# Kernel tuning notes

Measured on AMD Instinct MI355X. Metric: run time of the kernel, lower is better.

The kernel has to match this reference:

```python
import jax, jax.numpy as jnp
import numpy as np

B, C, H, W = 8, 256, 128, 128
HEADS, WS = 8, 8
SHIFT = WS // 2  # type=='W' -> shift_size = window_size//2 in this repo
N = WS * WS


def _rel_pos_index(ws):
    coords = np.stack(np.meshgrid(np.arange(ws), np.arange(ws), indexing='ij')).reshape(2, -1)
    rel = (coords[:, :, None] - coords[:, None, :]).transpose(1, 2, 0)  # N,N,2
    rel[:, :, 0] += ws - 1
    rel[:, :, 1] += ws - 1
    rel[:, :, 0] *= 2 * ws - 1
    return rel.sum(-1)  # (N,N) ints in [0,(2ws-1)^2)


def _attn_mask(h, w, ws, shift):
    img = np.zeros((h, w), np.int32)
    cnt = 0
    for hs in (slice(0, -ws), slice(-ws, -shift), slice(-shift, None)):
        for wsl in (slice(0, -ws), slice(-ws, -shift), slice(-shift, None)):
            img[hs, wsl] = cnt
            cnt += 1
    m = img.reshape(h // ws, ws, w // ws, ws).transpose(0, 2, 1, 3).reshape(-1, ws * ws)
    diff = m[:, None, :] - m[:, :, None]
    return np.where(diff != 0, -100.0, 0.0).astype(np.float32)  # (nW,N,N)


def _ln(x, w, b, eps=1e-5):
    mu = jnp.mean(x, -1, keepdims=True)
    var = jnp.mean(jnp.square(x - mu), -1, keepdims=True)
    return (x - mu) * jax.lax.rsqrt(var + eps) * w + b


def setup_inputs() -> dict:
    key = jax.random.key(0)
    ks = jax.random.split(key, 10)
    s = 0.02
    return {
        'x': jax.random.normal(ks[0], (B, C, H, W), jnp.float32),
        'ln1_w': jnp.ones((C,), jnp.float32),
        'ln1_b': jnp.zeros((C,), jnp.float32),
        'qkv_w': jax.random.normal(ks[1], (3 * C, C), jnp.float32) * s,
        'qkv_b': jnp.zeros((3 * C,), jnp.float32),
        'rel_bias': jax.random.normal(ks[2], ((2 * WS - 1) ** 2, HEADS), jnp.float32) * s,
        'proj_w': jax.random.normal(ks[3], (C, C), jnp.float32) * s,
        'proj_b': jnp.zeros((C,), jnp.float32),
        'ln2_w': jnp.ones((C,), jnp.float32),
        'ln2_b': jnp.zeros((C,), jnp.float32),
        'fc1_w': jax.random.normal(ks[4], (4 * C, C), jnp.float32) * s,
        'fc1_b': jnp.zeros((4 * C,), jnp.float32),
        'fc2_w': jax.random.normal(ks[5], (C, 4 * C), jnp.float32) * s,
        'fc2_b': jnp.zeros((C,), jnp.float32),
    }


def reference(x, ln1_w, ln1_b, qkv_w, qkv_b, rel_bias, proj_w, proj_b,
              ln2_w, ln2_b, fc1_w, fc1_b, fc2_w, fc2_b):
    b, c, h, w = x.shape
    hd = c // HEADS
    scale = hd ** -0.5
    nW = (h // WS) * (w // WS)

    t = x.transpose(0, 2, 3, 1).reshape(b, h * w, c)  # b (hw) c
    shortcut = t
    t = _ln(t, ln1_w, ln1_b).reshape(b, h, w, c)
    t = jnp.roll(t, (-SHIFT, -SHIFT), axis=(1, 2))  # cyclic shift
    # window partition -> (b*nW, N, c)
    win = t.reshape(b, h // WS, WS, w // WS, WS, c).transpose(0, 1, 3, 2, 4, 5).reshape(b * nW, N, c)

    qkv = (win @ qkv_w.T + qkv_b).reshape(b * nW, N, 3, HEADS, hd).transpose(2, 0, 3, 1, 4)
    q, k, v = qkv[0], qkv[1], qkv[2]  # (b*nW, heads, N, hd)
    attn = jnp.einsum('bhnd,bhmd->bhnm', q * scale, k)
    rpi = jnp.asarray(_rel_pos_index(WS))
    bias = rel_bias[rpi.reshape(-1)].reshape(N, N, HEADS).transpose(2, 0, 1)  # (heads,N,N)
    attn = attn + bias[None]
    mask = jnp.asarray(_attn_mask(h, w, WS, SHIFT))  # (nW,N,N)
    attn = attn.reshape(b, nW, HEADS, N, N) + mask[None, :, None]
    attn = jax.nn.softmax(attn, axis=-1).reshape(b * nW, HEADS, N, N)
    out = jnp.einsum('bhnm,bhmd->bhnd', attn, v).transpose(0, 2, 1, 3).reshape(b * nW, N, c)
    out = out @ proj_w.T + proj_b
    # window reverse + reverse shift
    out = out.reshape(b, h // WS, w // WS, WS, WS, c).transpose(0, 1, 3, 2, 4, 5).reshape(b, h, w, c)
    out = jnp.roll(out, (SHIFT, SHIFT), axis=(1, 2)).reshape(b, h * w, c)

    t = shortcut + out
    h2 = _ln(t, ln2_w, ln2_b)
    h2 = jax.nn.gelu(h2 @ fc1_w.T + fc1_b)
    t = t + (h2 @ fc2_w.T + fc2_b)
    return t.reshape(b, h, w, c).transpose(0, 3, 1, 2)
```

## Files before the change

### kernel.cpp

```cpp
#include <hip/hip_runtime.h>
#include <cstdint>
#include <cstddef>

using f32x4 = __attribute__((ext_vector_type(4))) float;
using bf16x8 = __attribute__((ext_vector_type(8))) __bf16;
using u16x4 = __attribute__((ext_vector_type(4))) unsigned short;
using u16x8 = __attribute__((ext_vector_type(8))) unsigned short;

#define DEV __device__ __forceinline__

DEV unsigned short f2b(float f) {
  __bf16 h = (__bf16)f;
  return __builtin_bit_cast(unsigned short, h);
}
DEV float b2f(unsigned short u) {
  uint32_t w = ((uint32_t)u) << 16;
  return __builtin_bit_cast(float, w);
}

DEV void gload16(const unsigned short* g, unsigned short* l) {
  __builtin_amdgcn_global_load_lds(
      (const __attribute__((address_space(1))) void*)g,
      (__attribute__((address_space(3))) void*)l, 16, 0, 0);
}

DEV void waitv(int n) {
  switch (n) {
    case 0: asm volatile("s_waitcnt vmcnt(0)" ::: "memory"); break;
    case 3: asm volatile("s_waitcnt vmcnt(3)" ::: "memory"); break;
    case 4: asm volatile("s_waitcnt vmcnt(4)" ::: "memory"); break;
    case 8: asm volatile("s_waitcnt vmcnt(8)" ::: "memory"); break;
    default: asm volatile("s_waitcnt vmcnt(0)" ::: "memory"); break;
  }
}


__global__ void swin_cvt_all(const float* __restrict__ qkvw, const float* __restrict__ projw,
                             const float* __restrict__ fc1w, const float* __restrict__ fc2w,
                             unsigned short* __restrict__ wq, unsigned short* __restrict__ wp,
                             unsigned short* __restrict__ w1, unsigned short* __restrict__ w2) {
  int i = blockIdx.x * 256 + threadIdx.x;
  if (i < 196608) wq[i] = f2b(qkvw[i]);
  else if (i < 262144) wp[i - 196608] = f2b(projw[i - 196608]);
  else if (i < 524288) w1[i - 262144] = f2b(fc1w[i - 262144]);
  else w2[i - 524288] = f2b(fc2w[i - 524288]);
}

__global__ void swin_btab(const float* __restrict__ relb, float* __restrict__ bt) {
  int id = blockIdx.x * 256 + threadIdx.x;
  int m = id & 63, n = (id >> 6) & 63, head = (id >> 12) & 7, cls = id >> 15;
  bool eh = cls & 2, ew = cls & 1;
  int nh = n >> 3, nw = n & 7, mh = m >> 3, mw = m & 7;
  int rn = (eh ? ((nh >> 2) + 1) : 0) * 3 + (ew ? ((nw >> 2) + 1) : 0);
  int rm = (eh ? ((mh >> 2) + 1) : 0) * 3 + (ew ? ((mw >> 2) + 1) : 0);
  float v = relb[(size_t)((nh - mh + 7) * 15 + (nw - mw + 7)) * 8 + head];
  if (rn != rm) v -= 100.f;
  bt[id] = v;
}

__global__ __launch_bounds__(256)
void swin_ln1win(const float* __restrict__ x,
                 const float* __restrict__ lw, const float* __restrict__ lb,
                 unsigned short* __restrict__ win, unsigned short* __restrict__ xb) {
  __shared__ float sh[512];
  __shared__ float mean_[128], rstd_[128];
  __shared__ unsigned short tile[128 * 136];
  int bh = blockIdx.x; int b = bh >> 7, h = bh & 127;
  int t = threadIdx.x;
  int w = t & 127, ch = t >> 7;
  const float* px = x + (((size_t)(b * 256 + ch * 128)) << 14) + (h << 7) + w;
  float s = 0.f, s2 = 0.f;
  for (int c = 0; c < 128; ++c) {
    float v = px[(size_t)c << 14];
    s += v; s2 += v * v;
  }
  sh[t] = s; sh[256 + t] = s2;
  __syncthreads();
  if (ch == 0) {
    s += sh[t + 128]; s2 += sh[256 + t + 128];
    float mu = s * (1.f / 256.f);
    mean_[w] = mu;
    rstd_[w] = rsqrtf(s2 * (1.f / 256.f) - mu * mu + 1e-5f);
  }
  int hp = (h + 124) & 127;
  int whh = hp >> 3, nh = hp & 7;
  int lg = t & 31, grp = t >> 5;
#pragma unroll
  for (int half = 0; half < 2; ++half) {
    int c0 = half << 7;
    __syncthreads();
#pragma unroll
    for (int i = 0; i < 64; ++i) {
      int cr = (i << 1) + ch;
      float v = x[(((size_t)(b * 256 + c0 + cr)) << 14) + (h << 7) + w];
      tile[w * 136 + cr] = f2b(v);
    }
    __syncthreads();
#pragma unroll
    for (int i = 0; i < 16; ++i) {
      int w2 = (i << 3) + grp;
      u16x4 raw = *(const u16x4*)&tile[w2 * 136 + (lg << 2)];
      float mu = mean_[w2], rs = rstd_[w2];
      int c = c0 + (lg << 2);
      f32x4 lwv = *(const f32x4*)(lw + c);
      f32x4 lbv = *(const f32x4*)(lb + c);
      u16x4 o;
#pragma unroll
      for (int k = 0; k < 4; ++k)
        o[k] = f2b((b2f(raw[k]) - mu) * rs * lwv[k] + lbv[k]);
      int wp_ = (w2 + 124) & 127;
      int wwc = wp_ >> 3, nw = wp_ & 7;
      size_t wt = (size_t)b * 256 + whh * 16 + wwc;
      int n = (nh << 3) + nw;
      *(u16x4*)&win[((wt << 6) + n) * 256 + c] = o;
      *(u16x4*)&xb[(((size_t)bh << 7) + w2) * 256 + c] = raw;
    }
  }
}

__global__ __launch_bounds__(512)
void swin_qkvattn(const unsigned short* __restrict__ win,
                  const unsigned short* __restrict__ wq,
                  const float* __restrict__ qkvb,
                  const float* __restrict__ btab,
                  unsigned short* __restrict__ attn_out) {
  __shared__ __align__(16) char L[133120];
  const int wt = blockIdx.x;
  const int t = threadIdx.x;
  const int lane = t & 63;
  const int head = t >> 6;
  const int cl = lane & 15, g = lane >> 4;

  {
    const unsigned short* src = win + (size_t)wt * 16384;
    int row = t >> 3;
    int sch = (t & 7) ^ (row & 7);
#pragma unroll
    for (int o = 0; o < 4; ++o)
      gload16(src + row * 256 + o * 64 + sch * 8,
              (unsigned short*)(L + o * 8192 + t * 16));
  }
  __syncthreads();

  f32x4 acc1[4][6] = {};
#pragma unroll
  for (int kt = 0; kt < 8; ++kt) {
    bf16x8 af[4], bf[6];
    const char* sub = L + (kt >> 1) * 8192;
    const int kc = (kt & 1) * 4 + g;
#pragma unroll
    for (int i = 0; i < 4; ++i) {
      int tok = i * 16 + cl;
      af[i] = *(const bf16x8*)(sub + tok * 128 + ((kc ^ (tok & 7)) * 16));
    }
#pragma unroll
    for (int j = 0; j < 6; ++j) {
      int col = (j >> 1) * 256 + head * 32 + (j & 1) * 16 + cl;
      bf[j] = *(const bf16x8*)(wq + (size_t)col * 256 + kt * 32 + g * 8);
    }
#pragma unroll
    for (int i = 0; i < 4; ++i)
#pragma unroll
      for (int j = 0; j < 6; ++j)
        acc1[i][j] = __builtin_amdgcn_mfma_f32_16x16x32_bf16(bf[j], af[i], acc1[i][j], 0, 0, 0);
  }

  char* hb = L + 32768 + head * 12544;
#pragma unroll
  for (int i = 0; i < 4; ++i) {
    int tok = i * 16 + cl;
#pragma unroll
    for (int j = 0; j < 6; ++j) {
      int p = j >> 1;
      int c32b = (j & 1) * 16 + (g << 2);
      f32x4 b4 = *(const f32x4*)(qkvb + p * 256 + head * 32 + c32b);
      if (p < 2) {
        u16x4 o;
#pragma unroll
        for (int r = 0; r < 4; ++r) {
          float v = acc1[i][j][r] + b4[r];
          if (p == 0) v *= 0.17677669529663687f;
          o[r] = f2b(v);
        }
        int chunk = ((j & 1) * 2 + (g >> 1)) ^ ((tok >> 1) & 3);
        *(u16x4*)(hb + p * 4096 + tok * 64 + chunk * 16 + (g & 1) * 8) = o;
      } else {
        unsigned short* vt = (unsigned short*)(hb + 8192);
#pragma unroll
        for (int r = 0; r < 4; ++r)
          vt[(c32b + r) * 68 + tok] = f2b(acc1[i][j][r] + b4[r]);
      }
    }
  }
  asm volatile("s_waitcnt lgkmcnt(0)" ::: "memory");
  __builtin_amdgcn_sched_barrier(0);

  bf16x8 qf[4], kf[4];
#pragma unroll
  for (int ni = 0; ni < 4; ++ni) {
    int tok = (ni << 4) + cl;
    int chunk = g ^ ((tok >> 1) & 3);
    qf[ni] = *(const bf16x8*)(hb + tok * 64 + chunk * 16);
    kf[ni] = *(const bf16x8*)(hb + 4096 + tok * 64 + chunk * 16);
  }
  f32x4 s[4][4] = {};
#pragma unroll
  for (int mi = 0; mi < 4; ++mi)
#pragma unroll
    for (int ni = 0; ni < 4; ++ni)
      s[mi][ni] = __builtin_amdgcn_mfma_f32_16x16x32_bf16(kf[mi], qf[ni], s[mi][ni], 0, 0, 0);

  int wi = wt & 255;
  int cls = (((wi >> 4) == 15) ? 2 : 0) + (((wi & 15) == 15) ? 1 : 0);
  const float* bt = btab + (((size_t)(cls << 3) + head) << 12);
#pragma unroll
  for (int ni = 0; ni < 4; ++ni) {
    int n = (ni << 4) + cl;
    float mx = -1e30f;
#pragma unroll
    for (int mi = 0; mi < 4; ++mi) {
      f32x4 bb = *(const f32x4*)&bt[n * 64 + (mi << 4) + (g << 2)];
#pragma unroll
      for (int r = 0; r < 4; ++r) {
        float v = s[mi][ni][r] + bb[r];
        s[mi][ni][r] = v;
        mx = fmaxf(mx, v);
      }
    }
    mx = fmaxf(mx, __shfl_xor(mx, 16));
    mx = fmaxf(mx, __shfl_xor(mx, 32));
    float sum = 0.f;
#pragma unroll
    for (int mi = 0; mi < 4; ++mi)
#pragma unroll
      for (int r = 0; r < 4; ++r) {
        float p = __expf(s[mi][ni][r] - mx);
        s[mi][ni][r] = p;
        sum += p;
      }
    sum += __shfl_xor(sum, 16);
    sum += __shfl_xor(sum, 32);
    float inv = __builtin_amdgcn_rcpf(sum);
#pragma unroll
    for (int mi = 0; mi < 4; ++mi) {
      u16x4 pk;
#pragma unroll
      for (int r = 0; r < 4; ++r) pk[r] = f2b(s[mi][ni][r] * inv);
      int chunk = (mi * 2 + (g >> 1)) ^ (n & 7);
      *(u16x4*)(hb + n * 128 + chunk * 16 + (g & 1) * 8) = pk;
    }
  }
  asm volatile("s_waitcnt lgkmcnt(0)" ::: "memory");
  __builtin_amdgcn_sched_barrier(0);

  union FragU { bf16x8 v; uint64_t q[2]; };
  f32x4 o[4][2] = {};
  const unsigned short* vt = (const unsigned short*)(hb + 8192);
#pragma unroll
  for (int mt = 0; mt < 2; ++mt) {
    FragU vf[2];
#pragma unroll
    for (int dt = 0; dt < 2; ++dt) {
      int d = (dt << 4) + cl;
      const unsigned short* p = vt + d * 68 + (mt << 5) + (g << 3);
      vf[dt].q[0] = *(const uint64_t*)p;
      vf[dt].q[1] = *(const uint64_t*)(p + 4);
    }
#pragma unroll
    for (int ni = 0; ni < 4; ++ni) {
      int n = (ni << 4) + cl;
      int chunk = (mt * 4 + g) ^ (n & 7);
      bf16x8 pa = *(const bf16x8*)(hb + n * 128 + chunk * 16);
#pragma unroll
      for (int dt = 0; dt < 2; ++dt)
        o[ni][dt] = __builtin_amdgcn_mfma_f32_16x16x32_bf16(pa, vf[dt].v, o[ni][dt], 0, 0, 0);
    }
  }

  int b = wt >> 8;
#pragma unroll
  for (int ni = 0; ni < 4; ++ni)
#pragma unroll
    for (int dt = 0; dt < 2; ++dt)
#pragma unroll
      for (int r = 0; r < 4; ++r) {
        int n = (ni << 4) + (g << 2) + r;
        int d = (dt << 4) + cl;
        int hs = ((wi >> 4) << 3) + (n >> 3), ws_ = ((wi & 15) << 3) + (n & 7);
        int hh = (hs + 4) & 127, ww = (ws_ + 4) & 127;
        size_t tok = ((size_t)b << 14) + (hh << 7) + ww;
        attn_out[tok * 256 + (head << 5) + d] = f2b(o[ni][dt][r]);
      }
}

__global__ __launch_bounds__(512, 2)
void swin_proj(const unsigned short* __restrict__ A,
               const unsigned short* __restrict__ Wt,
               const float* __restrict__ bias,
               unsigned short* __restrict__ T,
               const unsigned short* __restrict__ xb,
               const float* __restrict__ lw2, const float* __restrict__ lb2,
               unsigned short* __restrict__ tn) {
  constexpr int KT = 4;
  __shared__ __align__(16) unsigned short As[2][16384];
  __shared__ __align__(16) unsigned short Bs[2][16384];
  const int cpx = gridDim.x >> 3;
  const int bid = (blockIdx.x & 7) * cpx + (blockIdx.x >> 3);
  const int m0 = bid << 8;
  const int t = threadIdx.x;
  const int lane = t & 63;
  const int wave = t >> 6;
  const int wr = wave >> 2, wc = wave & 3;
  const int cl = lane & 15, g = lane >> 4;

  const int trow = t >> 3;
  const int ks = (t & 7) ^ (trow & 7);
  const unsigned short* agb = A  + (size_t)(m0 + trow) * 256 + ks * 8;
  const unsigned short* bgb = Wt + (size_t)trow * 256 + ks * 8;

  const int ra = wr * 128 + cl;
  const int rb = wc * 64 + cl;
  const int ka0 = (g ^ (cl & 7)) * 8;

  auto stage = [&](int buf, int kt) {
    const int ko = kt * 64;
#pragma unroll
    for (int l = 0; l < 4; ++l) {
      gload16(agb + (size_t)l * 64 * 256 + ko, &As[buf][l * 4096 + t * 8]);
      gload16(bgb + (size_t)l * 64 * 256 + ko, &Bs[buf][l * 4096 + t * 8]);
    }
  };

  f32x4 acc[8][4] = {};
  bf16x8 afA[8], bfA[4], afB[8], bfB[4];

  auto RD = [&](int buf, int kk, bf16x8* af, bf16x8* bfr) {
    const int ka = ka0 ^ (kk << 5);
#pragma unroll
    for (int i = 0; i < 8; ++i)
      af[i] = *(const bf16x8*)&As[buf][(ra + i * 16) * 64 + ka];
#pragma unroll
    for (int j = 0; j < 4; ++j)
      bfr[j] = *(const bf16x8*)&Bs[buf][(rb + j * 16) * 64 + ka];
  };
  auto MF = [&](bf16x8* af, bf16x8* bfr) {
    __builtin_amdgcn_s_setprio(1);
#pragma unroll
    for (int i = 0; i < 8; ++i)
#pragma unroll
      for (int j = 0; j < 4; ++j)
        acc[i][j] = __builtin_amdgcn_mfma_f32_16x16x32_bf16(bfr[j], af[i], acc[i][j], 0, 0, 0);
    __builtin_amdgcn_s_setprio(0);
  };

  stage(0, 0);
  stage(1, 1);
  waitv(8);
  __builtin_amdgcn_s_barrier();
  RD(0, 0, afA, bfA);
#pragma unroll
  for (int kt = 0; kt < KT; ++kt) {
    const int cur = kt & 1;
    RD(cur, 1, afB, bfB);
    MF(afA, bfA);
    asm volatile("s_waitcnt lgkmcnt(0)" ::: "memory");
    __builtin_amdgcn_sched_barrier(0);
    __builtin_amdgcn_s_barrier();
    if (kt + 2 < KT) stage(cur, kt + 2);
    if (kt + 1 < KT) waitv(8);
    else             waitv(0);
    __builtin_amdgcn_s_barrier();
    if (kt + 1 < KT) RD(cur ^ 1, 0, afA, bfA);
    MF(afB, bfB);
  }

  float s[8], s2v[8];
#pragma unroll
  for (int i = 0; i < 8; ++i) { s[i] = 0.f; s2v[i] = 0.f; }
#pragma unroll
  for (int i = 0; i < 8; ++i) {
    int row = m0 + wr * 128 + i * 16 + cl;
#pragma unroll
    for (int j = 0; j < 4; ++j) {
      int colb = wc * 64 + j * 16 + (g << 2);
      f32x4 b4 = *(const f32x4*)(bias + colb);
      u16x4 xv = *(const u16x4*)(xb + (size_t)row * 256 + colb);
#pragma unroll
      for (int r = 0; r < 4; ++r) {
        float v = acc[i][j][r] + b4[r] + b2f(xv[r]);
        acc[i][j][r] = v;
        s[i] += v; s2v[i] += v * v;
      }
    }
  }
#pragma unroll
  for (int i = 0; i < 8; ++i) {
    s[i]  += __shfl_xor(s[i], 16);  s[i]  += __shfl_xor(s[i], 32);
    s2v[i] += __shfl_xor(s2v[i], 16); s2v[i] += __shfl_xor(s2v[i], 32);
  }
  __syncthreads();
  float* lsum = (float*)&As[0][0];
  if (g == 0) {
#pragma unroll
    for (int i = 0; i < 8; ++i) {
      int rl = wr * 128 + i * 16 + cl;
      lsum[wc * 256 + rl] = s[i];
      lsum[1024 + wc * 256 + rl] = s2v[i];
    }
  }
  __syncthreads();
#pragma unroll
  for (int i = 0; i < 8; ++i) {
    int rl = wr * 128 + i * 16 + cl;
    float ts = lsum[rl] + lsum[256 + rl] + lsum[512 + rl] + lsum[768 + rl];
    float ts2 = lsum[1024 + rl] + lsum[1280 + rl] + lsum[1536 + rl] + lsum[1792 + rl];
    float mu = ts * (1.f / 256.f);
    float rstd = rsqrtf(ts2 * (1.f / 256.f) - mu * mu + 1e-5f);
    int row = m0 + rl;
#pragma unroll
    for (int j = 0; j < 4; ++j) {
      int colb = wc * 64 + j * 16 + (g << 2);
      f32x4 wv = *(const f32x4*)(lw2 + colb);
      f32x4 bv = *(const f32x4*)(lb2 + colb);
      u16x4 oT, on;
#pragma unroll
      for (int r = 0; r < 4; ++r) {
        float v = acc[i][j][r];
        oT[r] = f2b(v);
        on[r] = f2b((v - mu) * rstd * wv[r] + bv[r]);
      }
      *(u16x4*)(T + (size_t)row * 256 + colb) = oT;
      *(u16x4*)(tn + (size_t)row * 256 + colb) = on;
    }
  }
}

__global__ __launch_bounds__(512)
void swin_ffn(const unsigned short* __restrict__ tn,
              const unsigned short* __restrict__ w1,
              const unsigned short* __restrict__ w2,
              const float* __restrict__ b1,
              const float* __restrict__ b2,
              const unsigned short* __restrict__ T,
              float* __restrict__ out) {
  __shared__ __align__(16) unsigned short As[2][4096];
  __shared__ __align__(16) unsigned short Bs[2][16384];
  __shared__ __align__(16) unsigned short Hs[32768];
  const int cpx = gridDim.x >> 3;
  const int bid = (blockIdx.x & 7) * cpx + (blockIdx.x >> 3);
  const int m0 = bid << 7;
  const int t = threadIdx.x;
  const int lane = t & 63;
  const int wave = t >> 6;
  const int wr = wave >> 2, wc = wave & 3;
  const int cl = lane & 15, g = lane >> 4;

  const int arow = t >> 2;
  const int ks = (t & 3) ^ ((arow >> 1) & 3);
  const unsigned short* ag = tn + (size_t)(m0 + arow) * 256 + ks * 8;

  const int ka = (g ^ ((cl >> 1) & 3)) * 8;
  const int ra = wr * 64 + cl;
  const int rb = wc * 64 + cl;
  const int brow = t >> 3;
  const int bch = (t & 7) ^ (brow & 7);

  auto stage1 = [&](int buf, int q, int kt) {
    gload16(ag + kt * 32, &As[buf][t * 8]);
    const unsigned short* wg = w1 + (size_t)(q * 256 + arow) * 256 + kt * 32 + ks * 8;
    gload16(wg, &Bs[buf][t * 8]);
    gload16(wg + 32768, &Bs[buf][4096 + t * 8]);
  };
  auto stage2 = [&](int buf, int q, int kt) {
#pragma unroll
    for (int l = 0; l < 4; ++l) {
      const unsigned short* wg = w2 + (size_t)(l * 64 + brow) * 1024 + q * 256 + kt * 64 + bch * 8;
      gload16(wg, &Bs[buf][l * 4096 + t * 8]);
    }
  };

  f32x4 acc2[4][4] = {};

  for (int q = 0; q < 4; ++q) {
    f32x4 acc1[4][4] = {};
    stage1(0, q, 0); stage1(1, q, 1);
#pragma unroll
    for (int kt = 0; kt < 8; ++kt) {
      const int cur = kt & 1;
      waitv(kt < 7 ? 3 : 0);
      __builtin_amdgcn_s_barrier();
      bf16x8 af[4], bf[4];
#pragma unroll
      for (int i = 0; i < 4; ++i)
        af[i] = *(const bf16x8*)&As[cur][(ra + i * 16) * 32 + ka];
#pragma unroll
      for (int j = 0; j < 4; ++j)
        bf[j] = *(const bf16x8*)&Bs[cur][(rb + j * 16) * 32 + ka];
      asm volatile("s_waitcnt lgkmcnt(0)" ::: "memory");
      __builtin_amdgcn_sched_barrier(0);
      __builtin_amdgcn_s_barrier();
      if (kt + 2 < 8) stage1(cur, q, kt + 2);
      __builtin_amdgcn_s_setprio(1);
#pragma unroll
      for (int i = 0; i < 4; ++i)
#pragma unroll
        for (int j = 0; j < 4; ++j)
          acc1[i][j] = __builtin_amdgcn_mfma_f32_16x16x32_bf16(bf[j], af[i], acc1[i][j], 0, 0, 0);
      __builtin_amdgcn_s_setprio(0);
    }
    stage2(0, q, 0); stage2(1, q, 1);
#pragma unroll
    for (int i = 0; i < 4; ++i) {
      int row = wr * 64 + i * 16 + cl;
#pragma unroll
      for (int j = 0; j < 4; ++j) {
        f32x4 b4 = *(const f32x4*)(b1 + q * 256 + wc * 64 + j * 16 + (g << 2));
        u16x4 o;
#pragma unroll
        for (int r = 0; r < 4; ++r) {
          float v = acc1[i][j][r] + b4[r];
          float p = v * fmaf(v * v, -0.0713548256f, -1.5957691216f);
          float e = __expf(p);
          o[r] = f2b(v * __builtin_amdgcn_rcpf(1.f + e));
        }
        int chunk = (j * 2 + (g >> 1)) ^ (row & 7);
        *(u16x4*)((char*)Hs + wc * 16384 + row * 128 + chunk * 16 + (g & 1) * 8) = o;
      }
    }
    asm volatile("s_waitcnt lgkmcnt(0)" ::: "memory");
    __builtin_amdgcn_sched_barrier(0);
    __builtin_amdgcn_s_barrier();
#pragma unroll
    for (int kt = 0; kt < 4; ++kt) {
      const int cur = kt & 1;
      waitv(kt < 3 ? 4 : 0);
      __builtin_amdgcn_s_barrier();
      bf16x8 af2[4][2], bf2[4][2];
#pragma unroll
      for (int i = 0; i < 4; ++i) {
        int row = ra + i * 16;
#pragma unroll
        for (int kk = 0; kk < 2; ++kk)
          af2[i][kk] = *(const bf16x8*)((const char*)Hs + kt * 16384 + row * 128 +
                                        (((kk * 4 + g) ^ (row & 7)) * 16));
      }
#pragma unroll
      for (int j = 0; j < 4; ++j) {
        int row = rb + j * 16;
#pragma unroll
        for (int kk = 0; kk < 2; ++kk)
          bf2[j][kk] = *(const bf16x8*)&Bs[cur][row * 64 + (((kk * 4 + g) ^ (cl & 7)) * 8)];
      }
      asm volatile("s_waitcnt lgkmcnt(0)" ::: "memory");
      __builtin_amdgcn_sched_barrier(0);
      __builtin_amdgcn_s_barrier();
      if (kt + 2 < 4) stage2(cur, q, kt + 2);
      __builtin_amdgcn_s_setprio(1);
#pragma unroll
      for (int kk = 0; kk < 2; ++kk)
#pragma unroll
        for (int i = 0; i < 4; ++i)
#pragma unroll
          for (int j = 0; j < 4; ++j)
            acc2[i][j] = __builtin_amdgcn_mfma_f32_16x16x32_bf16(bf2[j][kk], af2[i][kk],
                                                                 acc2[i][j], 0, 0, 0);
      __builtin_amdgcn_s_setprio(0);
    }
  }

#pragma unroll
  for (int i = 0; i < 4; ++i) {
    int row = m0 + wr * 64 + i * 16 + cl;
    int b = row >> 14, hw = row & 16383;
#pragma unroll
    for (int j = 0; j < 4; ++j) {
      int colb = wc * 64 + j * 16 + (g << 2);
      f32x4 b4 = *(const f32x4*)(b2 + colb);
      u16x4 tv = *(const u16x4*)(T + (size_t)row * 256 + colb);
#pragma unroll
      for (int r = 0; r < 4; ++r)
        out[((size_t)(b * 256 + colb + r) << 14) + hw] = acc2[i][j][r] + b4[r] + b2f(tv[r]);
    }
  }
}

extern "C" void kernel_launch(void* const* d_in, const int* in_sizes, int n_in,
                              void* d_out, int out_size, void* d_ws, size_t ws_size,
                              hipStream_t stream) {
  const float* x    = (const float*)d_in[0];
  const float* ln1w = (const float*)d_in[1];
  const float* ln1b = (const float*)d_in[2];
  const float* qkvw = (const float*)d_in[3];
  const float* qkvb = (const float*)d_in[4];
  const float* relb = (const float*)d_in[5];
  const float* projw = (const float*)d_in[6];
  const float* projb = (const float*)d_in[7];
  const float* ln2w = (const float*)d_in[8];
  const float* ln2b = (const float*)d_in[9];
  const float* fc1w = (const float*)d_in[10];
  const float* fc1b = (const float*)d_in[11];
  const float* fc2w = (const float*)d_in[12];
  const float* fc2b = (const float*)d_in[13];

  char* ws = (char*)d_ws;
  unsigned short* win      = (unsigned short*)(ws);
  unsigned short* attn_out = (unsigned short*)(ws + 67108864);
  unsigned short* tn       = (unsigned short*)(ws + 134217728);
  unsigned short* T        = (unsigned short*)(ws + 268435456);
  unsigned short* xb       = (unsigned short*)(ws + 335544320);
  unsigned short* wq  = (unsigned short*)(ws + 402653184);
  unsigned short* wp  = (unsigned short*)(ws + 403046400);
  unsigned short* w1  = (unsigned short*)(ws + 403177472);
  unsigned short* w2  = (unsigned short*)(ws + 403701760);
  float* btab         = (float*)(ws + 404226048);

  if (ws_size < 404750336ull) return;

  swin_cvt_all<<<3072, 256, 0, stream>>>(qkvw, projw, fc1w, fc2w, wq, wp, w1, w2);
  swin_btab<<<512, 256, 0, stream>>>(relb, btab);
  swin_ln1win<<<1024, 256, 0, stream>>>(x, ln1w, ln1b, win, xb);
  swin_qkvattn<<<2048, 512, 0, stream>>>(win, wq, qkvb, btab, attn_out);
  swin_proj<<<512, 512, 0, stream>>>(attn_out, wp, projb, T, xb, ln2w, ln2b, tn);
  swin_ffn<<<1024, 512, 0, stream>>>(tn, w1, w2, fc1b, fc2b, T, (float*)d_out);
}
```

Measured before the change: 539.8 us.

## Keep FFN activation tile resident in LDS, fuse btab launch, single-pass LN1 read

The FFN kernel now loads its 128x256 input activation tile into LDS once, instead of restreaming it for each of the four hidden quarters. It also restructures the fc2 weight staging into smaller 32-wide K steps with two loads each. The bias-table kernel is merged into the weight-conversion kernel to save a launch. LN1 now reads x only once, staging bf16 values into a wider LDS tile during the statistics pass. The larger LDS footprint may reduce occupancy, and the finer fc2 K-steps add more barriers.

```diff
diff --git a/kernel.cpp b/kernel.cpp
--- a/kernel.cpp
+++ b/kernel.cpp
@@ -27,8 +27,7 @@
 DEV void waitv(int n) {
   switch (n) {
     case 0: asm volatile("s_waitcnt vmcnt(0)" ::: "memory"); break;
-    case 3: asm volatile("s_waitcnt vmcnt(3)" ::: "memory"); break;
-    case 4: asm volatile("s_waitcnt vmcnt(4)" ::: "memory"); break;
+    case 2: asm volatile("s_waitcnt vmcnt(2)" ::: "memory"); break;
     case 8: asm volatile("s_waitcnt vmcnt(8)" ::: "memory"); break;
     default: asm volatile("s_waitcnt vmcnt(0)" ::: "memory"); break;
   }
@@ -38,24 +37,24 @@
 __global__ void swin_cvt_all(const float* __restrict__ qkvw, const float* __restrict__ projw,
                              const float* __restrict__ fc1w, const float* __restrict__ fc2w,
                              unsigned short* __restrict__ wq, unsigned short* __restrict__ wp,
-                             unsigned short* __restrict__ w1, unsigned short* __restrict__ w2) {
+                             unsigned short* __restrict__ w1, unsigned short* __restrict__ w2,
+                             const float* __restrict__ relb, float* __restrict__ bt) {
   int i = blockIdx.x * 256 + threadIdx.x;
   if (i < 196608) wq[i] = f2b(qkvw[i]);
   else if (i < 262144) wp[i - 196608] = f2b(projw[i - 196608]);
   else if (i < 524288) w1[i - 262144] = f2b(fc1w[i - 262144]);
-  else w2[i - 524288] = f2b(fc2w[i - 524288]);
-}
-
-__global__ void swin_btab(const float* __restrict__ relb, float* __restrict__ bt) {
-  int id = blockIdx.x * 256 + threadIdx.x;
-  int m = id & 63, n = (id >> 6) & 63, head = (id >> 12) & 7, cls = id >> 15;
-  bool eh = cls & 2, ew = cls & 1;
-  int nh = n >> 3, nw = n & 7, mh = m >> 3, mw = m & 7;
-  int rn = (eh ? ((nh >> 2) + 1) : 0) * 3 + (ew ? ((nw >> 2) + 1) : 0);
-  int rm = (eh ? ((mh >> 2) + 1) : 0) * 3 + (ew ? ((mw >> 2) + 1) : 0);
-  float v = relb[(size_t)((nh - mh + 7) * 15 + (nw - mw + 7)) * 8 + head];
-  if (rn != rm) v -= 100.f;
-  bt[id] = v;
+  else if (i < 786432) w2[i - 524288] = f2b(fc2w[i - 524288]);
+  else {
+    int id = i - 786432;
+    int m = id & 63, n = (id >> 6) & 63, head = (id >> 12) & 7, cls = id >> 15;
+    bool eh = cls & 2, ew = cls & 1;
+    int nh = n >> 3, nw = n & 7, mh = m >> 3, mw = m & 7;
+    int rn = (eh ? ((nh >> 2) + 1) : 0) * 3 + (ew ? ((nw >> 2) + 1) : 0);
+    int rm = (eh ? ((mh >> 2) + 1) : 0) * 3 + (ew ? ((mw >> 2) + 1) : 0);
+    float v = relb[(size_t)((nh - mh + 7) * 15 + (nw - mw + 7)) * 8 + head];
+    if (rn != rm) v -= 100.f;
+    bt[id] = v;
+  }
 }
 
 __global__ __launch_bounds__(256)
@@ -64,7 +63,7 @@
                  unsigned short* __restrict__ win, unsigned short* __restrict__ xb) {
   __shared__ float sh[512];
   __shared__ float mean_[128], rstd_[128];
-  __shared__ unsigned short tile[128 * 136];
+  __shared__ unsigned short tile[128 * 260];
   int bh = blockIdx.x; int b = bh >> 7, h = bh & 127;
   int t = threadIdx.x;
   int w = t & 127, ch = t >> 7;
@@ -73,6 +72,7 @@
   for (int c = 0; c < 128; ++c) {
     float v = px[(size_t)c << 14];
     s += v; s2 += v * v;
+    tile[w * 260 + ch * 128 + c] = f2b(v);
   }
   sh[t] = s; sh[256 + t] = s2;
   __syncthreads();
@@ -82,36 +82,28 @@
     mean_[w] = mu;
     rstd_[w] = rsqrtf(s2 * (1.f / 256.f) - mu * mu + 1e-5f);
   }
+  __syncthreads();
   int hp = (h + 124) & 127;
   int whh = hp >> 3, nh = hp & 7;
   int lg = t & 31, grp = t >> 5;
 #pragma unroll
-  for (int half = 0; half < 2; ++half) {
-    int c0 = half << 7;
-    __syncthreads();
-#pragma unroll
-    for (int i = 0; i < 64; ++i) {
-      int cr = (i << 1) + ch;
-      float v = x[(((size_t)(b * 256 + c0 + cr)) << 14) + (h << 7) + w];
-      tile[w * 136 + cr] = f2b(v);
-    }
-    __syncthreads();
-#pragma unroll
-    for (int i = 0; i < 16; ++i) {
-      int w2 = (i << 3) + grp;
-      u16x4 raw = *(const u16x4*)&tile[w2 * 136 + (lg << 2)];
-      float mu = mean_[w2], rs = rstd_[w2];
-      int c = c0 + (lg << 2);
+  for (int i = 0; i < 16; ++i) {
+    int w2 = (i << 3) + grp;
+    float mu = mean_[w2], rs = rstd_[w2];
+    int wp_ = (w2 + 124) & 127;
+    int wwc = wp_ >> 3, nw = wp_ & 7;
+    size_t wt = (size_t)b * 256 + whh * 16 + wwc;
+    int n = (nh << 3) + nw;
+#pragma unroll
+    for (int half = 0; half < 2; ++half) {
+      int c = half * 128 + (lg << 2);
+      u16x4 raw = *(const u16x4*)&tile[w2 * 260 + c];
       f32x4 lwv = *(const f32x4*)(lw + c);
       f32x4 lbv = *(const f32x4*)(lb + c);
       u16x4 o;
 #pragma unroll
       for (int k = 0; k < 4; ++k)
         o[k] = f2b((b2f(raw[k]) - mu) * rs * lwv[k] + lbv[k]);
-      int wp_ = (w2 + 124) & 127;
-      int wwc = wp_ >> 3, nw = wp_ & 7;
-      size_t wt = (size_t)b * 256 + whh * 16 + wwc;
-      int n = (nh << 3) + nw;
       *(u16x4*)&win[((wt << 6) + n) * 256 + c] = o;
       *(u16x4*)&xb[(((size_t)bh << 7) + w2) * 256 + c] = raw;
     }
@@ -443,9 +435,9 @@
               const float* __restrict__ b2,
               const unsigned short* __restrict__ T,
               float* __restrict__ out) {
-  __shared__ __align__(16) unsigned short As[2][4096];
-  __shared__ __align__(16) unsigned short Bs[2][16384];
+  __shared__ __align__(16) unsigned short At[32768];
   __shared__ __align__(16) unsigned short Hs[32768];
+  __shared__ __align__(16) unsigned short Bs[2][8192];
   const int cpx = gridDim.x >> 3;
   const int bid = (blockIdx.x & 7) * cpx + (blockIdx.x >> 3);
   const int m0 = bid << 7;
@@ -457,49 +449,59 @@
 
   const int arow = t >> 2;
   const int ks = (t & 3) ^ ((arow >> 1) & 3);
-  const unsigned short* ag = tn + (size_t)(m0 + arow) * 256 + ks * 8;
-
   const int ka = (g ^ ((cl >> 1) & 3)) * 8;
   const int ra = wr * 64 + cl;
   const int rb = wc * 64 + cl;
-  const int brow = t >> 3;
-  const int bch = (t & 7) ^ (brow & 7);
-
-  auto stage1 = [&](int buf, int q, int kt) {
-    gload16(ag + kt * 32, &As[buf][t * 8]);
+
+  auto stageB1 = [&](int buf, int q, int kt) {
     const unsigned short* wg = w1 + (size_t)(q * 256 + arow) * 256 + kt * 32 + ks * 8;
     gload16(wg, &Bs[buf][t * 8]);
     gload16(wg + 32768, &Bs[buf][4096 + t * 8]);
   };
-  auto stage2 = [&](int buf, int q, int kt) {
-#pragma unroll
-    for (int l = 0; l < 4; ++l) {
-      const unsigned short* wg = w2 + (size_t)(l * 64 + brow) * 1024 + q * 256 + kt * 64 + bch * 8;
-      gload16(wg, &Bs[buf][l * 4096 + t * 8]);
-    }
+  auto stageB2 = [&](int buf, int q, int kt) {
+    const unsigned short* wg = w2 + (size_t)arow * 1024 + q * 256 + kt * 32 + ks * 8;
+    gload16(wg, &Bs[buf][t * 8]);
+    gload16(wg + 131072, &Bs[buf][4096 + t * 8]);
   };
+
+  {
+    int row0 = t >> 3;
+    int ch = t & 7;
+#pragma unroll
+    for (int o = 0; o < 4; ++o)
+#pragma unroll
+      for (int p = 0; p < 2; ++p) {
+        int row = p * 64 + row0;
+        int sch = ch ^ (row & 7);
+        gload16(tn + (size_t)(m0 + row) * 256 + o * 64 + sch * 8,
+                &At[o * 8192 + (p * 512 + t) * 8]);
+      }
+  }
 
   f32x4 acc2[4][4] = {};
 
   for (int q = 0; q < 4; ++q) {
     f32x4 acc1[4][4] = {};
-    stage1(0, q, 0); stage1(1, q, 1);
+    stageB1(0, q, 0); stageB1(1, q, 1);
 #pragma unroll
     for (int kt = 0; kt < 8; ++kt) {
       const int cur = kt & 1;
-      waitv(kt < 7 ? 3 : 0);
+      waitv(kt < 7 ? 2 : 0);
       __builtin_amdgcn_s_barrier();
       bf16x8 af[4], bf[4];
 #pragma unroll
-      for (int i = 0; i < 4; ++i)
-        af[i] = *(const bf16x8*)&As[cur][(ra + i * 16) * 32 + ka];
+      for (int i = 0; i < 4; ++i) {
+        int row = ra + i * 16;
+        int kc = ((kt & 1) * 4 + g) ^ (row & 7);
+        af[i] = *(const bf16x8*)&At[(kt >> 1) * 8192 + row * 64 + kc * 8];
+      }
 #pragma unroll
       for (int j = 0; j < 4; ++j)
         bf[j] = *(const bf16x8*)&Bs[cur][(rb + j * 16) * 32 + ka];
       asm volatile("s_waitcnt lgkmcnt(0)" ::: "memory");
       __builtin_amdgcn_sched_barrier(0);
       __builtin_amdgcn_s_barrier();
-      if (kt + 2 < 8) stage1(cur, q, kt + 2);
+      if (kt + 2 < 8) stageB1(cur, q, kt + 2);
       __builtin_amdgcn_s_setprio(1);
 #pragma unroll
       for (int i = 0; i < 4; ++i)
@@ -508,7 +510,7 @@
           acc1[i][j] = __builtin_amdgcn_mfma_f32_16x16x32_bf16(bf[j], af[i], acc1[i][j], 0, 0, 0);
       __builtin_amdgcn_s_setprio(0);
     }
-    stage2(0, q, 0); stage2(1, q, 1);
+    stageB2(0, q, 0); stageB2(1, q, 1);
 #pragma unroll
     for (int i = 0; i < 4; ++i) {
       int row = wr * 64 + i * 16 + cl;
@@ -531,39 +533,30 @@
     __builtin_amdgcn_sched_barrier(0);
     __builtin_amdgcn_s_barrier();
 #pragma unroll
-    for (int kt = 0; kt < 4; ++kt) {
+    for (int kt = 0; kt < 8; ++kt) {
       const int cur = kt & 1;
-      waitv(kt < 3 ? 4 : 0);
+      waitv(kt < 7 ? 2 : 0);
       __builtin_amdgcn_s_barrier();
-      bf16x8 af2[4][2], bf2[4][2];
+      bf16x8 af2[4], bf2[4];
 #pragma unroll
       for (int i = 0; i < 4; ++i) {
         int row = ra + i * 16;
-#pragma unroll
-        for (int kk = 0; kk < 2; ++kk)
-          af2[i][kk] = *(const bf16x8*)((const char*)Hs + kt * 16384 + row * 128 +
-                                        (((kk * 4 + g) ^ (row & 7)) * 16));
-      }
-#pragma unroll
-      for (int j = 0; j < 4; ++j) {
-        int row = rb + j * 16;
-#pragma unroll
-        for (int kk = 0; kk < 2; ++kk)
-          bf2[j][kk] = *(const bf16x8*)&Bs[cur][row * 64 + (((kk * 4 + g) ^ (cl & 7)) * 8)];
-      }
+        int kc = ((kt & 1) * 4 + g) ^ (row & 7);
+        af2[i] = *(const bf16x8*)&Hs[(kt >> 1) * 8192 + row * 64 + kc * 8];
+      }
+#pragma unroll
+      for (int j = 0; j < 4; ++j)
+        bf2[j] = *(const bf16x8*)&Bs[cur][(rb + j * 16) * 32 + ka];
       asm volatile("s_waitcnt lgkmcnt(0)" ::: "memory");
       __builtin_amdgcn_sched_barrier(0);
       __builtin_amdgcn_s_barrier();
-      if (kt + 2 < 4) stage2(cur, q, kt + 2);
+      if (kt + 2 < 8) stageB2(cur, q, kt + 2);
       __builtin_amdgcn_s_setprio(1);
 #pragma unroll
-      for (int kk = 0; kk < 2; ++kk)
-#pragma unroll
-        for (int i = 0; i < 4; ++i)
-#pragma unroll
-          for (int j = 0; j < 4; ++j)
-            acc2[i][j] = __builtin_amdgcn_mfma_f32_16x16x32_bf16(bf2[j][kk], af2[i][kk],
-                                                                 acc2[i][j], 0, 0, 0);
+      for (int i = 0; i < 4; ++i)
+#pragma unroll
+        for (int j = 0; j < 4; ++j)
+          acc2[i][j] = __builtin_amdgcn_mfma_f32_16x16x32_bf16(bf2[j], af2[i], acc2[i][j], 0, 0, 0);
       __builtin_amdgcn_s_setprio(0);
     }
   }
@@ -616,8 +609,7 @@
 
   if (ws_size < 404750336ull) return;
 
-  swin_cvt_all<<<3072, 256, 0, stream>>>(qkvw, projw, fc1w, fc2w, wq, wp, w1, w2);
-  swin_btab<<<512, 256, 0, stream>>>(relb, btab);
+  swin_cvt_all<<<3584, 256, 0, stream>>>(qkvw, projw, fc1w, fc2w, wq, wp, w1, w2, relb, btab);
   swin_ln1win<<<1024, 256, 0, stream>>>(x, ln1w, ln1b, win, xb);
   swin_qkvattn<<<2048, 512, 0, stream>>>(win, wq, qkvb, btab, attn_out);
   swin_proj<<<512, 512, 0, stream>>>(attn_out, wp, projb, T, xb, ln2w, ln2b, tn);
```

New measurement: 514.6 us. 4.7% less time.
